# Performance work log

Measured on AMD Instinct MI355X. Metric: run time of the kernel, lower is better.

## Reference

```python
import jax, jax.numpy as jnp
import numpy as np

BASE_K = 256
MAX_K = 512


def setup_inputs() -> dict:
    key = jax.random.key(0)
    kq, ks, kw, kb = jax.random.split(key, 4)
    B, S, D = 4, 4096, 1024
    Q = jax.random.normal(kq, (B, S, D), dtype=jnp.float32)
    scores = jax.random.normal(ks, (B, S, S), dtype=jnp.float32)
    # importance_net = nn.Linear(dim, 1): weight [1, dim], bias [1]
    bound = 1.0 / np.sqrt(D)
    W = jax.random.uniform(kw, (D,), dtype=jnp.float32, minval=-bound, maxval=bound)
    b = jax.random.uniform(kb, (1,), dtype=jnp.float32, minval=-bound, maxval=bound)
    return {"Q": Q, "scores": scores, "W": W, "b": b}


def reference(Q, scores, W, b):
    # importance gate: sigmoid(Linear(Q)) -> [B, S]
    importance = jax.nn.sigmoid(jnp.einsum("bsd,d->bs", Q, W) + b[0])
    # k per query; torch .long() truncates toward zero (values positive -> floor)
    k_per_query = (BASE_K + (MAX_K - BASE_K) * importance).astype(jnp.int32)
    # torch code does `indices, values = torch.topk(...)`, so the returned
    # 'indices' are actually the top-k VALUES. Reproduce faithfully.
    topk_values, _ = jax.lax.top_k(scores, MAX_K)  # [B, S, MAX_K]
    return topk_values, k_per_query
```

## Files before the change

kernel.cpp:

```cpp
#include <hip/hip_runtime.h>

#define SDIM 4096
#define DDIM 1024
#define NROWS 16384
#define KOUT 512
#define CAP 768

#define T0GUESS 0xBF800000u

__device__ __forceinline__ unsigned f2key(float f) {
    unsigned u = __float_as_uint(f);
    return (u & 0x80000000u) ? ~u : (u | 0x80000000u);
}
__device__ __forceinline__ float key2f(unsigned k) {
    unsigned u = (k & 0x80000000u) ? (k ^ 0x80000000u) : ~k;
    return __uint_as_float(u);
}
__device__ __forceinline__ unsigned lt_popc(unsigned long long m) {
    return __builtin_amdgcn_mbcnt_hi((unsigned)(m >> 32),
           __builtin_amdgcn_mbcnt_lo((unsigned)(m & 0xFFFFFFFFull), 0u));
}
__device__ __forceinline__ void wave_lds_fence() {
    asm volatile("s_waitcnt lgkmcnt(0)" ::: "memory");
}

__global__ __launch_bounds__(256, 1) void fused_kernel(
    const float* __restrict__ scores, const float* __restrict__ Q,
    const float* __restrict__ W, const float* __restrict__ bias,
    float* __restrict__ out_topk, float* __restrict__ out_k) {

    __shared__ unsigned cbuf[4][CAP];

    const int tid  = threadIdx.x;
    const int lane = tid & 63;
    const int wid  = tid >> 6;
    const int row  = blockIdx.x * 4 + wid;

    {
        const float4* q4 = (const float4*)(Q + (size_t)row * DDIM);
        const float4* w4 = (const float4*)W;
        float g = 0.f;
#pragma unroll
        for (int i = 0; i < 4; ++i) {
            float4 a = q4[lane + 64 * i];
            float4 b = w4[lane + 64 * i];
            g += a.x * b.x + a.y * b.y + a.z * b.z + a.w * b.w;
        }
#pragma unroll
        for (int off = 32; off; off >>= 1) g += __shfl_down(g, off, 64);
        if (lane == 0) {
            float x   = g + bias[0];
            float imp = 1.0f / (1.0f + expf(-x));
            out_k[row] = (float)(int)(256.0f + 256.0f * imp);
        }
    }

    unsigned key[64];
    {
        const float4* src = (const float4*)(scores + (size_t)row * SDIM);
#pragma unroll
        for (int i = 0; i < 16; ++i) {
            float4 v = src[lane + 64 * i];
            key[4 * i + 0] = f2key(v.x);
            key[4 * i + 1] = f2key(v.y);
            key[4 * i + 2] = f2key(v.z);
            key[4 * i + 3] = f2key(v.w);
        }
    }

    unsigned cnt = 0;
    {
#pragma unroll
        for (int i = 0; i < 64; ++i) {
            bool p = key[i] >= T0GUESS;
            unsigned long long m = __ballot(p);
            unsigned a = cnt + lt_popc(m);
            if (p && a < CAP) cbuf[wid][a] = key[i];
            cnt += (unsigned)__popcll(m);
        }
    }

    unsigned T;
    unsigned mtot = 0;
    bool have = (cnt >= (unsigned)KOUT) && (cnt <= (unsigned)CAP);

    if (!have) {
        unsigned prefix = 0;
        unsigned tot    = SDIM;
        bool     trig   = false;
#pragma unroll 1
        for (int b = 31; b >= 0; --b) {
            const unsigned candk = prefix | (1u << b);
            unsigned total = 0;
#pragma unroll
            for (int i = 0; i < 64; ++i)
                total += (unsigned)__popcll(__ballot(key[i] >= candk));
            if (total >= (unsigned)KOUT) {
                prefix = candk;
                tot    = total;
                if (total <= (unsigned)CAP) { trig = true; break; }
            }
        }
        if (trig) {
            cnt  = tot;
            have = true;
            unsigned c = 0;
#pragma unroll
            for (int i = 0; i < 64; ++i) {
                bool p = key[i] >= prefix;
                unsigned long long m = __ballot(p);
                unsigned a = c + lt_popc(m);
                if (p && a < CAP) cbuf[wid][a] = key[i];
                c += (unsigned)__popcll(m);
            }
        } else {
            T = prefix;
#pragma unroll
            for (int i = 0; i < 64; ++i) {
                bool p = key[i] > T;
                unsigned long long m = __ballot(p);
                if (p) cbuf[wid][mtot + lt_popc(m)] = key[i];
                mtot += (unsigned)__popcll(m);
            }
        }
    }

    if (have) {
        wave_lds_fence();

        unsigned ck[12];
#pragma unroll
        for (int j = 0; j < 12; ++j) {
            unsigned idx = (unsigned)lane + 64u * (unsigned)j;
            unsigned v = cbuf[wid][idx];
            ck[j] = (idx < cnt) ? v : 0u;
        }

        unsigned pfx = 0;
        if (cnt > (unsigned)KOUT) {
#pragma unroll 1
            for (int b = 31; b >= 0; --b) {
                const unsigned candk = pfx | (1u << b);
                unsigned total = 0;
#pragma unroll
                for (int j = 0; j < 12; ++j)
                    total += (unsigned)__popcll(__ballot(ck[j] >= candk));
                if (total >= (unsigned)KOUT) {
                    pfx = candk;
                    if (total == (unsigned)KOUT) break;
                }
            }
        }
        unsigned tmin = 0xFFFFFFFFu;
#pragma unroll
        for (int j = 0; j < 12; ++j) {
            unsigned t = (ck[j] >= pfx) ? ck[j] : 0xFFFFFFFFu;
            tmin = t < tmin ? t : tmin;
        }
#pragma unroll
        for (int off = 32; off; off >>= 1) {
            unsigned o = __shfl_xor(tmin, off, 64);
            tmin = o < tmin ? o : tmin;
        }
        T = tmin;

#pragma unroll
        for (int j = 0; j < 12; ++j) {
            bool p = ck[j] > T;
            unsigned long long m = __ballot(p);
            if (p) cbuf[wid][mtot + lt_popc(m)] = ck[j];
            mtot += (unsigned)__popcll(m);
        }
    }

    wave_lds_fence();

    unsigned x[8];
#pragma unroll
    for (int r = 0; r < 8; ++r) {
        unsigned idx = 8 * (unsigned)lane + r;
        unsigned v = cbuf[wid][idx];
        x[r] = (idx < mtot) ? v : T;
    }

#pragma unroll
    for (int kk = 2; kk <= 512; kk <<= 1) {
#pragma unroll
        for (int j = kk >> 1; j >= 8; j >>= 1) {
            bool km = ((((8 * lane) & kk) == 0) == (((8 * lane) & j) == 0));
#pragma unroll
            for (int r = 0; r < 8; ++r) {
                unsigned p  = __shfl_xor(x[r], j >> 3, 64);
                unsigned mx = x[r] > p ? x[r] : p;
                unsigned mn = x[r] > p ? p : x[r];
                x[r] = km ? mx : mn;
            }
        }
#pragma unroll
        for (int j = (kk >> 1) < 4 ? (kk >> 1) : 4; j >= 1; j >>= 1) {
#pragma unroll
            for (int r = 0; r < 8; ++r) {
                if ((r & j) == 0) {
                    int rp = r | j;
                    unsigned a = x[r], b = x[rp];
                    bool d = (((8 * lane + r) & kk) == 0);
                    unsigned hi = a > b ? a : b;
                    unsigned lo = a > b ? b : a;
                    x[r]  = d ? hi : lo;
                    x[rp] = d ? lo : hi;
                }
            }
        }
    }

    float4* dst = (float4*)(out_topk + (size_t)row * KOUT);
    dst[2 * lane + 0] = make_float4(key2f(x[0]), key2f(x[1]), key2f(x[2]), key2f(x[3]));
    dst[2 * lane + 1] = make_float4(key2f(x[4]), key2f(x[5]), key2f(x[6]), key2f(x[7]));
}

extern "C" void kernel_launch(void* const* d_in, const int* in_sizes, int n_in,
                              void* d_out, int out_size, void* d_ws, size_t ws_size,
                              hipStream_t stream) {
    const float* Q      = (const float*)d_in[0];
    const float* scores = (const float*)d_in[1];
    const float* W      = (const float*)d_in[2];
    const float* b      = (const float*)d_in[3];
    float* out_topk = (float*)d_out;
    float* out_k    = (float*)d_out + (size_t)NROWS * KOUT;

    fused_kernel<<<NROWS / 4, 256, 0, stream>>>(scores, Q, W, b, out_topk, out_k);
}
```

Measured before the change: 425.7 us.

## Stream scores through ballot filter without register key array, raise occupancy

Removes the 64-element per-lane key array. Raw float bits are now filtered straight from the load with a signed-int compare against 1.0f, and the key transform is deferred to the candidates stored in LDS. The fallback radix-select paths re-read the row from global memory instead of keeping it in registers. The launch bound goes from 1 to 8 blocks per CU, so more waves can hide memory latency. The candidate radix select also skips bit levels that the candidates' min and max already decide. The trade-off is extra global traffic whenever the rare fallback paths run.

After: 426.2 us. Within noise of the previous version (+0.1%).

```diff
diff --git a/kernel.cpp b/kernel.cpp
--- a/kernel.cpp
+++ b/kernel.cpp
@@ -6,10 +6,9 @@
 #define KOUT 512
 #define CAP 768
 
-#define T0GUESS 0xBF800000u
-
-__device__ __forceinline__ unsigned f2key(float f) {
-    unsigned u = __float_as_uint(f);
+#define K0I 0x3F800000
+
+__device__ __forceinline__ unsigned kob(unsigned u) {
     return (u & 0x80000000u) ? ~u : (u | 0x80000000u);
 }
 __device__ __forceinline__ float key2f(unsigned k) {
@@ -24,7 +23,7 @@
     asm volatile("s_waitcnt lgkmcnt(0)" ::: "memory");
 }
 
-__global__ __launch_bounds__(256, 1) void fused_kernel(
+__global__ __launch_bounds__(256, 8) void fused_kernel(
     const float* __restrict__ scores, const float* __restrict__ Q,
     const float* __restrict__ W, const float* __restrict__ bias,
     float* __restrict__ out_topk, float* __restrict__ out_k) {
@@ -55,72 +54,84 @@
         }
     }
 
-    unsigned key[64];
-    {
-        const float4* src = (const float4*)(scores + (size_t)row * SDIM);
-#pragma unroll
-        for (int i = 0; i < 16; ++i) {
-            float4 v = src[lane + 64 * i];
-            key[4 * i + 0] = f2key(v.x);
-            key[4 * i + 1] = f2key(v.y);
-            key[4 * i + 2] = f2key(v.z);
-            key[4 * i + 3] = f2key(v.w);
-        }
-    }
+    const uint4* src = (const uint4*)(scores + (size_t)row * SDIM);
+
+#define FUSE_ELEM(u) do {                                   \
+        bool p = (int)(u) >= K0I;                           \
+        unsigned long long m = __ballot(p);                 \
+        unsigned a = cnt + lt_popc(m);                      \
+        if (p && a < CAP) cbuf[wid][a] = (u);               \
+        cnt += (unsigned)__popcll(m);                       \
+    } while (0)
 
     unsigned cnt = 0;
-    {
-#pragma unroll
-        for (int i = 0; i < 64; ++i) {
-            bool p = key[i] >= T0GUESS;
-            unsigned long long m = __ballot(p);
-            unsigned a = cnt + lt_popc(m);
-            if (p && a < CAP) cbuf[wid][a] = key[i];
-            cnt += (unsigned)__popcll(m);
-        }
-    }
-
-    unsigned T;
+#pragma unroll
+    for (int i = 0; i < 16; ++i) {
+        uint4 v = src[lane + 64 * i];
+        FUSE_ELEM(v.x); FUSE_ELEM(v.y); FUSE_ELEM(v.z); FUSE_ELEM(v.w);
+    }
+#undef FUSE_ELEM
+
+    unsigned T    = 0;
     unsigned mtot = 0;
     bool have = (cnt >= (unsigned)KOUT) && (cnt <= (unsigned)CAP);
 
     if (!have) {
-        unsigned prefix = 0;
-        unsigned tot    = SDIM;
-        bool     trig   = false;
+        unsigned prefix = 0, tot = 0;
+        bool trig = false;
 #pragma unroll 1
         for (int b = 31; b >= 0; --b) {
             const unsigned candk = prefix | (1u << b);
-            unsigned total = 0;
-#pragma unroll
-            for (int i = 0; i < 64; ++i)
-                total += (unsigned)__popcll(__ballot(key[i] >= candk));
-            if (total >= (unsigned)KOUT) {
-                prefix = candk;
-                tot    = total;
-                if (total <= (unsigned)CAP) { trig = true; break; }
+            const uint4* s2 = src;
+            asm volatile("" : "+v"(s2));
+            unsigned c = 0;
+#pragma unroll 1
+            for (int i = 0; i < 16; ++i) {
+                uint4 v = s2[lane + 64 * i];
+                c += (unsigned)(kob(v.x) >= candk) + (unsigned)(kob(v.y) >= candk)
+                   + (unsigned)(kob(v.z) >= candk) + (unsigned)(kob(v.w) >= candk);
+            }
+#pragma unroll
+            for (int off = 32; off; off >>= 1) c += __shfl_xor(c, off, 64);
+            if (c >= (unsigned)KOUT) {
+                prefix = candk; tot = c;
+                if (c <= (unsigned)CAP) { trig = true; break; }
             }
         }
         if (trig) {
-            cnt  = tot;
-            have = true;
+            const uint4* s2 = src;
+            asm volatile("" : "+v"(s2));
             unsigned c = 0;
-#pragma unroll
-            for (int i = 0; i < 64; ++i) {
-                bool p = key[i] >= prefix;
-                unsigned long long m = __ballot(p);
-                unsigned a = c + lt_popc(m);
-                if (p && a < CAP) cbuf[wid][a] = key[i];
-                c += (unsigned)__popcll(m);
-            }
+#pragma unroll 1
+            for (int i = 0; i < 16; ++i) {
+                uint4 v = s2[lane + 64 * i];
+                unsigned uu[4] = {v.x, v.y, v.z, v.w};
+#pragma unroll
+                for (int e = 0; e < 4; ++e) {
+                    bool p = kob(uu[e]) >= prefix;
+                    unsigned long long m = __ballot(p);
+                    unsigned a = c + lt_popc(m);
+                    if (p && a < CAP) cbuf[wid][a] = uu[e];
+                    c += (unsigned)__popcll(m);
+                }
+            }
+            cnt = tot; have = true;
         } else {
             T = prefix;
-#pragma unroll
-            for (int i = 0; i < 64; ++i) {
-                bool p = key[i] > T;
-                unsigned long long m = __ballot(p);
-                if (p) cbuf[wid][mtot + lt_popc(m)] = key[i];
-                mtot += (unsigned)__popcll(m);
+            const uint4* s2 = src;
+            asm volatile("" : "+v"(s2));
+#pragma unroll 1
+            for (int i = 0; i < 16; ++i) {
+                uint4 v = s2[lane + 64 * i];
+                unsigned uu[4] = {v.x, v.y, v.z, v.w};
+#pragma unroll
+                for (int e = 0; e < 4; ++e) {
+                    unsigned k = kob(uu[e]);
+                    bool p = k > T;
+                    unsigned long long m = __ballot(p);
+                    if (p) cbuf[wid][mtot + lt_popc(m)] = k;
+                    mtot += (unsigned)__popcll(m);
+                }
             }
         }
     }
@@ -129,11 +140,24 @@
         wave_lds_fence();
 
         unsigned ck[12];
+        unsigned mn = 0xFFFFFFFFu, mx = 0u;
 #pragma unroll
         for (int j = 0; j < 12; ++j) {
             unsigned idx = (unsigned)lane + 64u * (unsigned)j;
-            unsigned v = cbuf[wid][idx];
-            ck[j] = (idx < cnt) ? v : 0u;
+            unsigned u = cbuf[wid][idx];
+            unsigned k = kob(u);
+            bool val = idx < cnt;
+            ck[j] = val ? k : 0u;
+            unsigned km = val ? k : 0xFFFFFFFFu;
+            mn = km < mn ? km : mn;
+            mx = ck[j] > mx ? ck[j] : mx;
+        }
+#pragma unroll
+        for (int off = 32; off; off >>= 1) {
+            unsigned a = __shfl_xor(mn, off, 64);
+            unsigned b = __shfl_xor(mx, off, 64);
+            mn = a < mn ? a : mn;
+            mx = b > mx ? b : mx;
         }
 
         unsigned pfx = 0;
@@ -141,6 +165,8 @@
 #pragma unroll 1
             for (int b = 31; b >= 0; --b) {
                 const unsigned candk = pfx | (1u << b);
+                if (candk <= mn) { pfx = candk; continue; }
+                if (candk > mx) continue;
                 unsigned total = 0;
 #pragma unroll
                 for (int j = 0; j < 12; ++j)
@@ -191,9 +217,9 @@
 #pragma unroll
             for (int r = 0; r < 8; ++r) {
                 unsigned p  = __shfl_xor(x[r], j >> 3, 64);
-                unsigned mx = x[r] > p ? x[r] : p;
-                unsigned mn = x[r] > p ? p : x[r];
-                x[r] = km ? mx : mn;
+                unsigned mx2 = x[r] > p ? x[r] : p;
+                unsigned mn2 = x[r] > p ? p : x[r];
+                x[r] = km ? mx2 : mn2;
             }
         }
 #pragma unroll
```
